# Performance work log

Measured on AMD Instinct MI355X. Metric: run time of the kernel, lower is better.

## Reference

```python
import jax, jax.numpy as jnp
import numpy as np

B, T, C = 4, 2048, 768
N_HEAD = 12
HS = C // N_HEAD

def setup_inputs() -> dict:
    key = jax.random.key(0)
    ks = jax.random.split(key, 5)
    s = 0.02
    return {
        "x": jax.random.normal(ks[0], (B, T, C), dtype=jnp.float32),
        "w_attn": jax.random.normal(ks[1], (C, 3 * C), dtype=jnp.float32) * s,
        "b_attn": jnp.zeros((3 * C,), dtype=jnp.float32),
        "w_proj": jax.random.normal(ks[2], (C, C), dtype=jnp.float32) * s,
        "b_proj": jnp.zeros((C,), dtype=jnp.float32),
    }

def reference(x, w_attn, b_attn, w_proj, b_proj):
    Bx, Tx, Cx = x.shape
    qkv = x @ w_attn + b_attn                      # [B,T,3C]
    q, k, v = jnp.split(qkv, 3, axis=-1)
    # [B,H,T,hs]
    q = q.reshape(Bx, Tx, N_HEAD, HS).transpose(0, 2, 1, 3)
    k = k.reshape(Bx, Tx, N_HEAD, HS).transpose(0, 2, 1, 3)
    v = v.reshape(Bx, Tx, N_HEAD, HS).transpose(0, 2, 1, 3)
    att = jnp.einsum('bhqd,bhkd->bhqk', q, k) * (1.0 / jnp.sqrt(jnp.float32(HS)))
    mask = jnp.tril(jnp.ones((Tx, Tx), dtype=bool))  # causal
    att = jnp.where(mask, att, jnp.float32(-jnp.inf))
    att = jax.nn.softmax(att, axis=-1)
    y = jnp.einsum('bhqk,bhkd->bhqd', att, v)
    y = y.transpose(0, 2, 1, 3).reshape(Bx, Tx, Cx)
    return y @ w_proj + b_proj
```

## Files before the change

### kernel.cpp

```cpp
#include <hip/hip_runtime.h>

#define BB 4
#define TT 2048
#define CC 768
#define QKVW 2304
#define NHH 12
#define HSS 64
#define NQT64 (TT / 64)

typedef __attribute__((ext_vector_type(4))) float floatx4;
typedef __attribute__((ext_vector_type(8))) short shortx8;
typedef __attribute__((ext_vector_type(4))) short shortx4;

__device__ __forceinline__ unsigned short f2bf(float f) {
  union { float f; unsigned int u; } cv; cv.f = f;
  unsigned int u = cv.u;
  u += 0x7FFFu + ((u >> 16) & 1u);
  return (unsigned short)(u >> 16);
}
__device__ __forceinline__ unsigned short bfp(float f) {
  union { float f; unsigned int u; } cv; cv.f = f;
  return (unsigned short)((cv.u + 0x8000u) >> 16);
}
__device__ __forceinline__ unsigned short bft(float f) {
  union { float f; unsigned int u; } cv; cv.f = f;
  return (unsigned short)(cv.u >> 16);
}

__device__ __forceinline__ void async_copy16(const void* g, void* l) {
  __builtin_amdgcn_global_load_lds(
      (const __attribute__((address_space(1))) unsigned int*)g,
      (__attribute__((address_space(3))) unsigned int*)l, 16, 0, 0);
}

__device__ __forceinline__ floatx4 mfma16(shortx4 a, shortx4 b, floatx4 c) {
  return __builtin_amdgcn_mfma_f32_16x16x16bf16_1k(a, b, c, 0, 0, 0);
}

__global__ void convert_x(const float* __restrict__ x, unsigned short* __restrict__ xb, int n4) {
  int i = blockIdx.x * blockDim.x + threadIdx.x;
  const int stride = gridDim.x * blockDim.x;
  for (; i < n4; i += stride) {
    float4 v = ((const float4*)x)[i];
    shortx4 s;
    s.x = (short)f2bf(v.x); s.y = (short)f2bf(v.y);
    s.z = (short)f2bf(v.z); s.w = (short)f2bf(v.w);
    ((shortx4*)xb)[i] = s;
  }
}

__global__ __launch_bounds__(256)
void transpose_w(const float* __restrict__ w, unsigned short* __restrict__ wt, int K, int N) {
  __shared__ short tile[64 * 68];
  const int n0 = blockIdx.x * 64, k0 = blockIdx.y * 64;
  const int tid = threadIdx.x;
  {
    const int tr = tid >> 4, tc = (tid & 15) * 4;
#pragma unroll
    for (int i = 0; i < 4; ++i) {
      float4 v = *(const float4*)(w + (size_t)(k0 + tr + 16 * i) * N + n0 + tc);
      short* d = &tile[(tr + 16 * i) * 68 + tc];
      d[0] = (short)f2bf(v.x); d[1] = (short)f2bf(v.y);
      d[2] = (short)f2bf(v.z); d[3] = (short)f2bf(v.w);
    }
  }
  __syncthreads();
  {
    const int wr = tid >> 3, wc = (tid & 7) * 8;
#pragma unroll
    for (int j = 0; j < 2; ++j) {
      const int n = wr + 32 * j;
      shortx8 s;
#pragma unroll
      for (int e = 0; e < 8; ++e) s[e] = tile[(wc + e) * 68 + n];
      *(shortx8*)(wt + (size_t)(n0 + n) * K + k0 + wc) = s;
    }
  }
}

__global__ __launch_bounds__(256)
void transpose_v(const unsigned short* __restrict__ qkv, unsigned short* __restrict__ Vt) {
  __shared__ short tile[64 * 72];
  const int t0 = blockIdx.x * 64;
  const int bh = blockIdx.y;
  const int b = bh / NHH, h = bh % NHH;
  const int tid = threadIdx.x;
  {
    const int tr = tid >> 3, tc = (tid & 7) * 8;
#pragma unroll
    for (int i = 0; i < 2; ++i) {
      shortx8 v = *(const shortx8*)(qkv + ((size_t)(b * TT + t0 + tr + 32 * i)) * QKVW + 2 * CC + h * HSS + tc);
      *(shortx8*)&tile[(tr + 32 * i) * 72 + tc] = v;
    }
  }
  __syncthreads();
  {
    const int dr = tid >> 3, tc = (tid & 7) * 8;
#pragma unroll
    for (int j = 0; j < 2; ++j) {
      const int d = dr + 32 * j;
      shortx8 s;
#pragma unroll
      for (int e = 0; e < 8; ++e) s[e] = tile[(tc + e) * 72 + d];
      *(shortx8*)(Vt + ((size_t)bh * HSS + d) * TT + t0 + tc) = s;
    }
  }
}

template<bool OUT_BF16, bool QSCALE>
__global__ __launch_bounds__(256)
void gemm_tn(const unsigned short* __restrict__ A, const unsigned short* __restrict__ Bt,
             const float* __restrict__ bias, void* __restrict__ Cp, int M, int N, int K) {
  __shared__ short As0[128 * 32], As1[128 * 32];
  __shared__ short Bs0[128 * 32], Bs1[128 * 32];
  const int tid = threadIdx.x, lane = tid & 63, wave = tid >> 6;
  const int row = lane & 15, quad = lane >> 4;
  const int wm = (wave >> 1) * 64, wn = (wave & 1) * 64;
  const int m0 = blockIdx.x * 128, n0 = blockIdx.y * 128;

  floatx4 acc[4][4] = {};

  const int sr = wave * 32 + (lane >> 2);
  const int sc = (lane & 3) * 8;
  const unsigned short* aP = A + (size_t)(m0 + sr) * K + sc;
  const unsigned short* bP = Bt + (size_t)(n0 + sr) * K + sc;
  short* as0Base = &As0[(wave * 32) * 32];
  short* as1Base = &As1[(wave * 32) * 32];
  short* bs0Base = &Bs0[(wave * 32) * 32];
  short* bs1Base = &Bs1[(wave * 32) * 32];

  for (int k0 = 0; k0 < K; k0 += 64) {
#pragma unroll
    for (int i = 0; i < 2; ++i) {
      async_copy16(aP + (size_t)(16 * i) * K + k0,      as0Base + i * 512);
      async_copy16(aP + (size_t)(16 * i) * K + k0 + 32, as1Base + i * 512);
      async_copy16(bP + (size_t)(16 * i) * K + k0,      bs0Base + i * 512);
      async_copy16(bP + (size_t)(16 * i) * K + k0 + 32, bs1Base + i * 512);
    }
    __syncthreads();
    {
      shortx8 af[4], bf[4];
#pragma unroll
      for (int g = 0; g < 4; ++g) {
        af[g] = *(const shortx8*)&As0[(wm + g * 16 + row) * 32 + quad * 8];
        bf[g] = *(const shortx8*)&Bs0[(wn + g * 16 + row) * 32 + quad * 8];
      }
#pragma unroll
      for (int mg = 0; mg < 4; ++mg)
#pragma unroll
        for (int ng = 0; ng < 4; ++ng)
          acc[mg][ng] = __builtin_amdgcn_mfma_f32_16x16x32_bf16(af[mg], bf[ng], acc[mg][ng], 0, 0, 0);
#pragma unroll
      for (int g = 0; g < 4; ++g) {
        af[g] = *(const shortx8*)&As1[(wm + g * 16 + row) * 32 + quad * 8];
        bf[g] = *(const shortx8*)&Bs1[(wn + g * 16 + row) * 32 + quad * 8];
      }
#pragma unroll
      for (int mg = 0; mg < 4; ++mg)
#pragma unroll
        for (int ng = 0; ng < 4; ++ng)
          acc[mg][ng] = __builtin_amdgcn_mfma_f32_16x16x32_bf16(af[mg], bf[ng], acc[mg][ng], 0, 0, 0);
    }
    __syncthreads();
  }

#pragma unroll
  for (int mg = 0; mg < 4; ++mg) {
    const int m = m0 + wm + mg * 16 + quad * 4;
#pragma unroll
    for (int ng = 0; ng < 4; ++ng) {
      const int n = n0 + wn + ng * 16 + row;
      const float bv = bias[n];
      const float scl = (QSCALE && n < CC) ? 0.180336881f : 1.0f;
#pragma unroll
      for (int r = 0; r < 4; ++r) {
        const float val = (acc[mg][ng][r] + bv) * scl;
        if (OUT_BF16) ((unsigned short*)Cp)[(size_t)(m + r) * N + n] = f2bf(val);
        else          ((float*)Cp)[(size_t)(m + r) * N + n] = val;
      }
    }
  }
}

__global__ __launch_bounds__(256)
void attn_kernel(const unsigned short* __restrict__ qkv, const unsigned short* __restrict__ Vt,
                 unsigned short* __restrict__ y) {
  constexpr int STR = 72;
  __shared__ short Kd[2][64 * STR];
  __shared__ short Vd[2][64 * STR];

  const int p = blockIdx.x;
  const int h = blockIdx.y, b = blockIdx.z;
  const int bh = b * NHH + h;
  const int tid = threadIdx.x, lane = tid & 63, wave = tid >> 6;
  const int row = lane & 15, quad = lane >> 4;

  const int srow = tid >> 3;
  const int scol = (tid & 7) * 8;
  const unsigned short* kSrc = qkv + ((size_t)(b * TT)) * QKVW + CC + h * HSS;
  const unsigned short* vSrc = Vt + ((size_t)bh * HSS) * TT;

  const shortx4 ones = {(short)0x3F80, (short)0x3F80, (short)0x3F80, (short)0x3F80};

  for (int item = 0; item < 2; ++item) {
    const int qt = item == 0 ? (NQT64 - 1 - p) : p;
    const int qbase = qt * 64 + wave * 16;

    shortx8 qf0, qf1;
    {
      const unsigned short* qp = qkv + ((size_t)(b * TT) + qbase + row) * QKVW + h * HSS;
      qf0 = *(const shortx8*)(qp + quad * 8);
      qf1 = *(const shortx8*)(qp + 32 + quad * 8);
    }

    floatx4 lf = (floatx4)(0.0f);
    floatx4 o[4];
#pragma unroll
    for (int dg = 0; dg < 4; ++dg) o[dg] = (floatx4)(0.0f);

    shortx8 kr[2], vr[2];
#pragma unroll
    for (int i = 0; i < 2; ++i) {
      kr[i] = *(const shortx8*)(kSrc + (size_t)(srow + 32 * i) * QKVW + scol);
      vr[i] = *(const shortx8*)(vSrc + (size_t)(srow + 32 * i) * TT + scol);
    }
#pragma unroll
    for (int i = 0; i < 2; ++i) {
      *(shortx8*)&Kd[0][(srow + 32 * i) * STR + scol] = kr[i];
      *(shortx8*)&Vd[0][(srow + 32 * i) * STR + scol] = vr[i];
    }
    __syncthreads();

    const int nk = qt + 1;
    for (int kt = 0; kt < nk; ++kt) {
      const int cur = kt & 1;
      if (kt + 1 < nk) {
#pragma unroll
        for (int i = 0; i < 2; ++i) {
          kr[i] = *(const shortx8*)(kSrc + (size_t)((kt + 1) * 64 + srow + 32 * i) * QKVW + scol);
          vr[i] = *(const shortx8*)(vSrc + (size_t)(srow + 32 * i) * TT + (kt + 1) * 64 + scol);
        }
      }
      {
        const short* Kc = &Kd[cur][0];
        const short* Vc = &Vd[cur][0];
        floatx4 sa[4];
#pragma unroll
        for (int mg = 0; mg < 4; ++mg) {
          shortx8 kf0 = *(const shortx8*)&Kc[(mg * 16 + row) * STR + quad * 8];
          shortx8 kf1 = *(const shortx8*)&Kc[(mg * 16 + row) * STR + 32 + quad * 8];
          floatx4 t = __builtin_amdgcn_mfma_f32_16x16x32_bf16(kf0, qf0, (floatx4)(0.0f), 0, 0, 0);
          sa[mg] = __builtin_amdgcn_mfma_f32_16x16x32_bf16(kf1, qf1, t, 0, 0, 0);
        }
        if (kt == qt) {
#pragma unroll
          for (int mg = 0; mg < 4; ++mg) {
            const int kg = kt * 64 + mg * 16 + quad * 4;
#pragma unroll
            for (int r = 0; r < 4; ++r)
              if (kg + r > qbase + row) sa[mg][r] = -1e30f;
          }
        }
        shortx4 pfr[4];
#pragma unroll
        for (int mg = 0; mg < 4; ++mg) {
          shortx4 pk;
#pragma unroll
          for (int r = 0; r < 4; ++r)
            pk[r] = (short)bft(__builtin_amdgcn_exp2f(sa[mg][r]));
          pfr[mg] = pk;
        }
#pragma unroll
        for (int mg = 0; mg < 4; ++mg) {
          lf = mfma16(pfr[mg], ones, lf);
#pragma unroll
          for (int dg = 0; dg < 4; ++dg) {
            shortx4 vf = *(const shortx4*)&Vc[(dg * 16 + row) * STR + mg * 16 + quad * 4];
            o[dg] = mfma16(pfr[mg], vf, o[dg]);
          }
        }
      }
      if (kt + 1 < nk) {
        const int nb = (kt + 1) & 1;
#pragma unroll
        for (int i = 0; i < 2; ++i) {
          *(shortx8*)&Kd[nb][(srow + 32 * i) * STR + scol] = kr[i];
          *(shortx8*)&Vd[nb][(srow + 32 * i) * STR + scol] = vr[i];
        }
      }
      __syncthreads();
    }

    {
#pragma unroll
      for (int r = 0; r < 4; ++r) {
        const float lo = 1.0f / lf[r];
        unsigned short* yp = y + ((size_t)(b * TT) + qbase + quad * 4 + r) * CC + h * HSS;
#pragma unroll
        for (int dg = 0; dg < 4; ++dg)
          yp[dg * 16 + row] = bfp(o[dg][r] * lo);
      }
    }
  }
}

extern "C" void kernel_launch(void* const* d_in, const int* in_sizes, int n_in,
                              void* d_out, int out_size, void* d_ws, size_t ws_size,
                              hipStream_t stream) {
  const float* x      = (const float*)d_in[0];
  const float* w_attn = (const float*)d_in[1];
  const float* b_attn = (const float*)d_in[2];
  const float* w_proj = (const float*)d_in[3];
  const float* b_proj = (const float*)d_in[4];
  float* out = (float*)d_out;

  char* ws = (char*)d_ws;
  unsigned short* xb  = (unsigned short*)ws;
  unsigned short* y   = (unsigned short*)ws;
  unsigned short* qkv = (unsigned short*)(ws + 12582912);
  unsigned short* wta = (unsigned short*)(ws + 50331648);
  unsigned short* Vt  = (unsigned short*)(ws + 50331648);
  unsigned short* wtp = (unsigned short*)(ws + 62914560);

  const int M = BB * TT;

  convert_x<<<1024, 256, 0, stream>>>(x, xb, (M * CC) / 4);
  transpose_w<<<dim3(QKVW / 64, CC / 64), 256, 0, stream>>>(w_attn, wta, CC, QKVW);
  transpose_w<<<dim3(CC / 64, CC / 64), 256, 0, stream>>>(w_proj, wtp, CC, CC);

  gemm_tn<true, true><<<dim3(M / 128, QKVW / 128), 256, 0, stream>>>(
      xb, wta, b_attn, (void*)qkv, M, QKVW, CC);

  transpose_v<<<dim3(TT / 64, BB * NHH), 256, 0, stream>>>(qkv, Vt);

  attn_kernel<<<dim3(NQT64 / 2, NHH, BB), 256, 0, stream>>>(qkv, Vt, y);

  gemm_tn<false, false><<<dim3(M / 128, CC / 128), 256, 0, stream>>>(
      y, wtp, b_proj, (void*)out, M, CC, CC);
}
```

Baseline: 222.0 us.

## Process paired causal query tiles concurrently and use 16x16x32 MFMA for PV

The attention kernel no longer handles its two query tiles one after the other. Two waves take the long tile and two take the short tile, each wave covering 32 query rows, and all four share one pass over the K/V tiles. The PV and row-sum products switch from 16x16x16 to 16x16x32 MFMA, with the V transpose reordering columns so each P fragment pairs with contiguous 8-element V loads. This halves the number of K/V tile loads and sync loops per block and doubles K-fragment reuse per wave. The cost is more registers per wave and idle waves on the short side once its tiles are done.

```diff
diff --git a/kernel.cpp b/kernel.cpp
--- a/kernel.cpp
+++ b/kernel.cpp
@@ -31,10 +31,6 @@
   __builtin_amdgcn_global_load_lds(
       (const __attribute__((address_space(1))) unsigned int*)g,
       (__attribute__((address_space(3))) unsigned int*)l, 16, 0, 0);
-}
-
-__device__ __forceinline__ floatx4 mfma16(shortx4 a, shortx4 b, floatx4 c) {
-  return __builtin_amdgcn_mfma_f32_16x16x16bf16_1k(a, b, c, 0, 0, 0);
 }
 
 __global__ void convert_x(const float* __restrict__ x, unsigned short* __restrict__ xb, int n4) {
@@ -96,12 +92,14 @@
   __syncthreads();
   {
     const int dr = tid >> 3, tc = (tid & 7) * 8;
+    const int base = (tc & 32) + ((tc >> 3) & 3) * 4;
 #pragma unroll
     for (int j = 0; j < 2; ++j) {
       const int d = dr + 32 * j;
       shortx8 s;
 #pragma unroll
-      for (int e = 0; e < 8; ++e) s[e] = tile[(tc + e) * 72 + d];
+      for (int e = 0; e < 8; ++e)
+        s[e] = tile[(base + (e >> 2) * 16 + (e & 3)) * 72 + d];
       *(shortx8*)(Vt + ((size_t)bh * HSS + d) * TT + t0 + tc) = s;
     }
   }
@@ -195,111 +193,120 @@
   const int tid = threadIdx.x, lane = tid & 63, wave = tid >> 6;
   const int row = lane & 15, quad = lane >> 4;
 
+  const int side = wave >> 1;
+  const int qt = side ? p : (NQT64 - 1 - p);
+  const int qb0 = qt * 64 + (wave & 1) * 32;
+  const int nkS = qt + 1;
+  const int nk = NQT64 - p;
+
   const int srow = tid >> 3;
   const int scol = (tid & 7) * 8;
   const unsigned short* kSrc = qkv + ((size_t)(b * TT)) * QKVW + CC + h * HSS;
   const unsigned short* vSrc = Vt + ((size_t)bh * HSS) * TT;
 
-  const shortx4 ones = {(short)0x3F80, (short)0x3F80, (short)0x3F80, (short)0x3F80};
-
-  for (int item = 0; item < 2; ++item) {
-    const int qt = item == 0 ? (NQT64 - 1 - p) : p;
-    const int qbase = qt * 64 + wave * 16;
-
-    shortx8 qf0, qf1;
-    {
-      const unsigned short* qp = qkv + ((size_t)(b * TT) + qbase + row) * QKVW + h * HSS;
-      qf0 = *(const shortx8*)(qp + quad * 8);
-      qf1 = *(const shortx8*)(qp + 32 + quad * 8);
-    }
-
-    floatx4 lf = (floatx4)(0.0f);
-    floatx4 o[4];
-#pragma unroll
-    for (int dg = 0; dg < 4; ++dg) o[dg] = (floatx4)(0.0f);
-
-    shortx8 kr[2], vr[2];
-#pragma unroll
-    for (int i = 0; i < 2; ++i) {
-      kr[i] = *(const shortx8*)(kSrc + (size_t)(srow + 32 * i) * QKVW + scol);
-      vr[i] = *(const shortx8*)(vSrc + (size_t)(srow + 32 * i) * TT + scol);
-    }
-#pragma unroll
-    for (int i = 0; i < 2; ++i) {
-      *(shortx8*)&Kd[0][(srow + 32 * i) * STR + scol] = kr[i];
-      *(shortx8*)&Vd[0][(srow + 32 * i) * STR + scol] = vr[i];
+  const shortx8 ones8 = {(short)0x3F80, (short)0x3F80, (short)0x3F80, (short)0x3F80,
+                         (short)0x3F80, (short)0x3F80, (short)0x3F80, (short)0x3F80};
+
+  shortx8 qf[2][2];
+#pragma unroll
+  for (int qg = 0; qg < 2; ++qg) {
+    const unsigned short* qp = qkv + ((size_t)(b * TT) + qb0 + qg * 16 + row) * QKVW + h * HSS;
+    qf[qg][0] = *(const shortx8*)(qp + quad * 8);
+    qf[qg][1] = *(const shortx8*)(qp + 32 + quad * 8);
+  }
+
+  floatx4 lf[2] = {(floatx4)(0.0f), (floatx4)(0.0f)};
+  floatx4 o[2][4];
+#pragma unroll
+  for (int qg = 0; qg < 2; ++qg)
+#pragma unroll
+    for (int dg = 0; dg < 4; ++dg) o[qg][dg] = (floatx4)(0.0f);
+
+  shortx8 kr[2], vr[2];
+#pragma unroll
+  for (int i = 0; i < 2; ++i) {
+    kr[i] = *(const shortx8*)(kSrc + (size_t)(srow + 32 * i) * QKVW + scol);
+    vr[i] = *(const shortx8*)(vSrc + (size_t)(srow + 32 * i) * TT + scol);
+  }
+#pragma unroll
+  for (int i = 0; i < 2; ++i) {
+    *(shortx8*)&Kd[0][(srow + 32 * i) * STR + scol] = kr[i];
+    *(shortx8*)&Vd[0][(srow + 32 * i) * STR + scol] = vr[i];
+  }
+  __syncthreads();
+
+  for (int kt = 0; kt < nk; ++kt) {
+    const int cur = kt & 1;
+    if (kt + 1 < nk) {
+#pragma unroll
+      for (int i = 0; i < 2; ++i) {
+        kr[i] = *(const shortx8*)(kSrc + (size_t)((kt + 1) * 64 + srow + 32 * i) * QKVW + scol);
+        vr[i] = *(const shortx8*)(vSrc + (size_t)(srow + 32 * i) * TT + (kt + 1) * 64 + scol);
+      }
+    }
+    if (kt < nkS) {
+      const short* Kc = &Kd[cur][0];
+      const short* Vc = &Vd[cur][0];
+      shortx4 pfr[2][4];
+#pragma unroll
+      for (int mg = 0; mg < 4; ++mg) {
+        const shortx8 kf0 = *(const shortx8*)&Kc[(mg * 16 + row) * STR + quad * 8];
+        const shortx8 kf1 = *(const shortx8*)&Kc[(mg * 16 + row) * STR + 32 + quad * 8];
+#pragma unroll
+        for (int qg = 0; qg < 2; ++qg) {
+          floatx4 t = __builtin_amdgcn_mfma_f32_16x16x32_bf16(kf0, qf[qg][0], (floatx4)(0.0f), 0, 0, 0);
+          t = __builtin_amdgcn_mfma_f32_16x16x32_bf16(kf1, qf[qg][1], t, 0, 0, 0);
+          if (kt == qt) {
+            const int kg = kt * 64 + mg * 16 + quad * 4;
+            const int qv = qb0 + qg * 16 + row;
+#pragma unroll
+            for (int r = 0; r < 4; ++r)
+              if (kg + r > qv) t[r] = -1e30f;
+          }
+          shortx4 pk;
+#pragma unroll
+          for (int r = 0; r < 4; ++r) pk[r] = (short)bft(__builtin_amdgcn_exp2f(t[r]));
+          pfr[qg][mg] = pk;
+        }
+      }
+#pragma unroll
+      for (int kh = 0; kh < 2; ++kh) {
+        shortx8 pk8[2];
+#pragma unroll
+        for (int qg = 0; qg < 2; ++qg) {
+          pk8[qg] = __builtin_shufflevector(pfr[qg][2 * kh], pfr[qg][2 * kh + 1],
+                                            0, 1, 2, 3, 4, 5, 6, 7);
+          lf[qg] = __builtin_amdgcn_mfma_f32_16x16x32_bf16(pk8[qg], ones8, lf[qg], 0, 0, 0);
+        }
+#pragma unroll
+        for (int dg = 0; dg < 4; ++dg) {
+          const shortx8 vf = *(const shortx8*)&Vc[(dg * 16 + row) * STR + kh * 32 + quad * 8];
+#pragma unroll
+          for (int qg = 0; qg < 2; ++qg)
+            o[qg][dg] = __builtin_amdgcn_mfma_f32_16x16x32_bf16(pk8[qg], vf, o[qg][dg], 0, 0, 0);
+        }
+      }
+    }
+    if (kt + 1 < nk) {
+      const int nb = (kt + 1) & 1;
+#pragma unroll
+      for (int i = 0; i < 2; ++i) {
+        *(shortx8*)&Kd[nb][(srow + 32 * i) * STR + scol] = kr[i];
+        *(shortx8*)&Vd[nb][(srow + 32 * i) * STR + scol] = vr[i];
+      }
     }
     __syncthreads();
-
-    const int nk = qt + 1;
-    for (int kt = 0; kt < nk; ++kt) {
-      const int cur = kt & 1;
-      if (kt + 1 < nk) {
-#pragma unroll
-        for (int i = 0; i < 2; ++i) {
-          kr[i] = *(const shortx8*)(kSrc + (size_t)((kt + 1) * 64 + srow + 32 * i) * QKVW + scol);
-          vr[i] = *(const shortx8*)(vSrc + (size_t)(srow + 32 * i) * TT + (kt + 1) * 64 + scol);
-        }
-      }
-      {
-        const short* Kc = &Kd[cur][0];
-        const short* Vc = &Vd[cur][0];
-        floatx4 sa[4];
-#pragma unroll
-        for (int mg = 0; mg < 4; ++mg) {
-          shortx8 kf0 = *(const shortx8*)&Kc[(mg * 16 + row) * STR + quad * 8];
-          shortx8 kf1 = *(const shortx8*)&Kc[(mg * 16 + row) * STR + 32 + quad * 8];
-          floatx4 t = __builtin_amdgcn_mfma_f32_16x16x32_bf16(kf0, qf0, (floatx4)(0.0f), 0, 0, 0);
-          sa[mg] = __builtin_amdgcn_mfma_f32_16x16x32_bf16(kf1, qf1, t, 0, 0, 0);
-        }
-        if (kt == qt) {
-#pragma unroll
-          for (int mg = 0; mg < 4; ++mg) {
-            const int kg = kt * 64 + mg * 16 + quad * 4;
-#pragma unroll
-            for (int r = 0; r < 4; ++r)
-              if (kg + r > qbase + row) sa[mg][r] = -1e30f;
-          }
-        }
-        shortx4 pfr[4];
-#pragma unroll
-        for (int mg = 0; mg < 4; ++mg) {
-          shortx4 pk;
-#pragma unroll
-          for (int r = 0; r < 4; ++r)
-            pk[r] = (short)bft(__builtin_amdgcn_exp2f(sa[mg][r]));
-          pfr[mg] = pk;
-        }
-#pragma unroll
-        for (int mg = 0; mg < 4; ++mg) {
-          lf = mfma16(pfr[mg], ones, lf);
-#pragma unroll
-          for (int dg = 0; dg < 4; ++dg) {
-            shortx4 vf = *(const shortx4*)&Vc[(dg * 16 + row) * STR + mg * 16 + quad * 4];
-            o[dg] = mfma16(pfr[mg], vf, o[dg]);
-          }
-        }
-      }
-      if (kt + 1 < nk) {
-        const int nb = (kt + 1) & 1;
-#pragma unroll
-        for (int i = 0; i < 2; ++i) {
-          *(shortx8*)&Kd[nb][(srow + 32 * i) * STR + scol] = kr[i];
-          *(shortx8*)&Vd[nb][(srow + 32 * i) * STR + scol] = vr[i];
-        }
-      }
-      __syncthreads();
-    }
-
-    {
-#pragma unroll
-      for (int r = 0; r < 4; ++r) {
-        const float lo = 1.0f / lf[r];
-        unsigned short* yp = y + ((size_t)(b * TT) + qbase + quad * 4 + r) * CC + h * HSS;
-#pragma unroll
-        for (int dg = 0; dg < 4; ++dg)
-          yp[dg * 16 + row] = bfp(o[dg][r] * lo);
-      }
+  }
+
+#pragma unroll
+  for (int qg = 0; qg < 2; ++qg) {
+#pragma unroll
+    for (int r = 0; r < 4; ++r) {
+      const float lo = 1.0f / lf[qg][r];
+      unsigned short* yp = y + ((size_t)(b * TT) + qb0 + qg * 16 + quad * 4 + r) * CC + h * HSS;
+#pragma unroll
+      for (int dg = 0; dg < 4; ++dg)
+        yp[dg * 16 + row] = bfp(o[qg][dg][r] * lo);
     }
   }
 }
```

Result: slower. 267.2 us (+20.3%).
